# Kernel optimization log

Measured on AMD Instinct MI355X. Metric: run time of the kernel, lower is better.

## Reference

```python
import jax, jax.numpy as jnp
import numpy as np

N_NODES = 100000
N_EDGES = 1600000
IN_C, HID_C, OUT_C = 64, 64, 32


def gcn_conv(x, edge_index, W, b, n_nodes):
    """PyG GCNConv: add self-loops, symmetric norm, x @ W, scatter-add, + bias."""
    loop = jnp.arange(n_nodes, dtype=edge_index.dtype)
    src = jnp.concatenate([edge_index[0], loop])  # [E + N]
    dst = jnp.concatenate([edge_index[1], loop])
    # degree on destination (col) including self-loops -> deg >= 1
    deg = jax.ops.segment_sum(jnp.ones_like(dst, dtype=x.dtype), dst,
                              num_segments=n_nodes)
    dinv = jax.lax.rsqrt(deg)  # deg >= 1, no inf handling needed
    norm = dinv[src] * dinv[dst]  # [E + N]
    h = x @ W  # [N, C_out] -- transform first (small GEMM), then propagate
    msg = h[src] * norm[:, None]  # gather, memory-bound
    out = jax.ops.segment_sum(msg, dst, num_segments=n_nodes)  # scatter-add
    return out + b


def setup_inputs() -> dict:
    key = jax.random.key(0)
    k1, k2, k3, k4, k5 = jax.random.split(key, 5)
    x = jax.random.normal(k1, (N_NODES, IN_C), dtype=jnp.float32)
    edge_index = jax.random.randint(k2, (2, N_EDGES), 0, N_NODES, dtype=jnp.int64)
    s1 = 1.0 / np.sqrt(IN_C)
    s2 = 1.0 / np.sqrt(HID_C)
    W1 = jax.random.uniform(k3, (IN_C, HID_C), jnp.float32, -s1, s1)
    b1 = jnp.zeros((HID_C,), jnp.float32)
    W2 = jax.random.uniform(k4, (HID_C, OUT_C), jnp.float32, -s2, s2)
    b2 = jnp.zeros((OUT_C,), jnp.float32)
    return {"x": x, "edge_index": edge_index, "W1": W1, "b1": b1,
            "W2": W2, "b2": b2}


def reference(x, edge_index, W1, b1, W2, b2):
    n = x.shape[0]
    h = gcn_conv(x, edge_index, W1, b1, n)
    h = jax.nn.relu(h)
    out = gcn_conv(h, edge_index, W2, b2, n)
    return out
```

## Files before the change

kernel.cpp:

```cpp
#include <hip/hip_runtime.h>
#include <hip/hip_fp16.h>
#include <cstdint>
#include <cstddef>


#define CHUNK 4096
#define BKN 256
#define BKN_SHIFT 8
#define NCH_MAX 512
#define SCAP2 5120

__device__ __forceinline__ int load_edge(const int* e32, int idx, int is64) {
  if (is64) return (int)((const long long*)e32)[idx];
  return e32[idx];
}

__device__ __forceinline__ int detect_is64_block(const int* e32, int* s_tmp) {
  const int t = threadIdx.x;
  if (t < 64) {
    int v = e32[2 * t + 1];
    unsigned long long b = __ballot(v != 0);
    if (t == 0) *s_tmp = (b == 0ULL);
  }
  __syncthreads();
  return *s_tmp;
}

__global__ void k_histA(const int* __restrict__ e32, int E, int* __restrict__ histM,
                        int NBUCK) {
  __shared__ int lh[NCH_MAX];
  __shared__ int s_is64;
  const int c = blockIdx.x;
  const int t = threadIdx.x;
  const int is64 = detect_is64_block(e32, &s_is64);
  for (int i = t; i < NBUCK; i += 256) lh[i] = 0;
  __syncthreads();
  const int beg = c * CHUNK;
  const int n = min(CHUNK, E - beg);
  for (int i = t; i < n; i += 256) {
    int d = load_edge(e32, E + beg + i, is64);
    atomicAdd(&lh[d >> BKN_SHIFT], 1);
  }
  __syncthreads();
  for (int i = t; i < NBUCK; i += 256) histM[(size_t)c * NBUCK + i] = lh[i];
}

__device__ __forceinline__ void block_scan512(int* sh, int t) {
  for (int off = 1; off < 512; off <<= 1) {
    int i0 = t, i1 = t + 256;
    int v0 = sh[i0] + ((i0 >= off) ? sh[i0 - off] : 0);
    int v1 = sh[i1] + ((i1 >= off) ? sh[i1 - off] : 0);
    __syncthreads();
    sh[i0] = v0;
    sh[i1] = v1;
    __syncthreads();
  }
}

__global__ void k_colscanA(int* __restrict__ histM, int* __restrict__ btot,
                           int NCH, int NBUCK) {
  __shared__ int sh[NCH_MAX];
  const int b = blockIdx.x;
  const int t = threadIdx.x;
  for (int i = t; i < NCH_MAX; i += 256)
    sh[i] = (i < NCH) ? histM[(size_t)i * NBUCK + b] : 0;
  __syncthreads();
  block_scan512(sh, t);
  for (int i = t; i < NCH; i += 256)
    histM[(size_t)i * NBUCK + b] = (i == 0) ? 0 : sh[i - 1];
  if (t == 0) btot[b] = sh[NCH_MAX - 1];
}

__global__ void k_bscan(const int* __restrict__ btot, int* __restrict__ bbase,
                        int* __restrict__ rowptr, __half* __restrict__ h1,
                        __half* __restrict__ g1, __half* __restrict__ h2,
                        int NBUCK, int N, int E) {
  __shared__ int sh[NCH_MAX];
  const int t = threadIdx.x;
  sh[t] = (t < NBUCK) ? btot[t] : 0;
  sh[t + 256] = (t + 256 < NBUCK) ? btot[t + 256] : 0;
  __syncthreads();
  block_scan512(sh, t);
  for (int i = t; i < NBUCK; i += 256) bbase[i] = (i == 0) ? 0 : sh[i - 1];
  if (t == 0) { bbase[NBUCK] = E; rowptr[N] = E; }
  if (t < 64) {
    h1[(size_t)N * 64 + t] = __float2half(0.f);
    g1[(size_t)N * 64 + t] = __float2half(0.f);
    if (t < 32) h2[(size_t)N * 32 + t] = __float2half(0.f);
  }
}

__global__ void k_scatter(const int* __restrict__ e32, int E, const int* __restrict__ histM,
                          const int* __restrict__ bbase, int NBUCK,
                          unsigned int* __restrict__ raw) {
  __shared__ int lcur[NCH_MAX];
  __shared__ int s_is64;
  const int c = blockIdx.x;
  const int t = threadIdx.x;
  const int is64 = detect_is64_block(e32, &s_is64);
  for (int i = t; i < NBUCK; i += 256)
    lcur[i] = histM[(size_t)c * NBUCK + i] + bbase[i];
  __syncthreads();
  const int beg = c * CHUNK;
  const int cnt = min(CHUNK, E - beg);
  for (int i = t; i < cnt; i += 256) {
    int s = load_edge(e32, beg + i, is64);
    int d = load_edge(e32, E + beg + i, is64);
    int pos = atomicAdd(&lcur[d >> BKN_SHIFT], 1);
    raw[pos] = ((unsigned int)(d & (BKN - 1)) << 23) | (unsigned int)s;
  }
}

__global__ void k_sort(const unsigned int* __restrict__ raw, const int* __restrict__ bbase,
                       int* __restrict__ rec, int* __restrict__ rowptr,
                       float* __restrict__ dinv, int N) {
  __shared__ int srec[SCAP2];
  __shared__ int sh[BKN];
  const int b = blockIdx.x;
  const int t = threadIdx.x;
  const int nodebase = b << BKN_SHIFT;
  const int base = bbase[b];
  const int end = bbase[b + 1];
  const int count = end - base;
  sh[t] = 0;
  __syncthreads();
  for (int i = t; i < count; i += 256) atomicAdd(&sh[raw[base + i] >> 23], 1);
  __syncthreads();
  const int deg = sh[t];
  for (int off = 1; off < 256; off <<= 1) {
    int add = (t >= off) ? sh[t - off] : 0;
    __syncthreads();
    sh[t] += add;
    __syncthreads();
  }
  const int excl = sh[t] - deg;
  const int n = nodebase + t;
  if (n < N) {
    rowptr[n] = base + excl;
    dinv[n] = rsqrtf((float)deg + 1.0f);
  }
  __syncthreads();
  sh[t] = excl;
  __syncthreads();
  if (count <= SCAP2) {
    for (int i = t; i < count; i += 256) {
      unsigned int r = raw[base + i];
      int pos = atomicAdd(&sh[r >> 23], 1);
      srec[pos] = (int)(r & 0x7FFFFFu);
    }
    __syncthreads();
    for (int i = t; i < count; i += 256) rec[base + i] = srec[i];
  } else {
    for (int i = t; i < count; i += 256) {
      unsigned int r = raw[base + i];
      int pos = atomicAdd(&sh[r >> 23], 1);
      rec[base + pos] = (int)(r & 0x7FFFFFu);
    }
  }
}

template <int CIN, int COUT, bool IN16>
__global__ void k_gemm(const void* __restrict__ Xv, const float* __restrict__ W,
                       const float* __restrict__ dinv, __half* __restrict__ H, int N) {
  constexpr int Q = COUT / 4;
  constexpr int NODES = 256 / Q;
  __shared__ float4 Ws[CIN * Q];
  __shared__ float Xs[NODES][CIN + 1];
  const int t = threadIdx.x;
  const int nodebase = blockIdx.x * NODES;

  const float4* W4 = (const float4*)W;
#pragma unroll
  for (int i = t; i < CIN * Q; i += 256) Ws[i] = W4[i];

  if (IN16) {
    const __half2* X2 = (const __half2*)Xv;
#pragma unroll
    for (int i = t; i < NODES * (CIN / 2); i += 256) {
      int r = i / (CIN / 2);
      int k2 = i % (CIN / 2);
      int gr = nodebase + r;
      if (gr > N - 1) gr = N - 1;
      float2 f = __half22float2(X2[(size_t)gr * (CIN / 2) + k2]);
      Xs[r][k2 * 2 + 0] = f.x;
      Xs[r][k2 * 2 + 1] = f.y;
    }
  } else {
    const float4* X4 = (const float4*)Xv;
#pragma unroll
    for (int i = t; i < NODES * (CIN / 4); i += 256) {
      int r = i / (CIN / 4);
      int k4 = i % (CIN / 4);
      int gr = nodebase + r;
      if (gr > N - 1) gr = N - 1;
      float4 v = X4[(size_t)gr * (CIN / 4) + k4];
      Xs[r][k4 * 4 + 0] = v.x;
      Xs[r][k4 * 4 + 1] = v.y;
      Xs[r][k4 * 4 + 2] = v.z;
      Xs[r][k4 * 4 + 3] = v.w;
    }
  }
  __syncthreads();

  const int q = t % Q;
  const int nl = t / Q;
  const int n = nodebase + nl;
  float4 acc = make_float4(0.f, 0.f, 0.f, 0.f);
#pragma unroll 4
  for (int k = 0; k < CIN; ++k) {
    float xv = Xs[nl][k];
    float4 wv = Ws[k * Q + q];
    acc.x = fmaf(xv, wv.x, acc.x);
    acc.y = fmaf(xv, wv.y, acc.y);
    acc.z = fmaf(xv, wv.z, acc.z);
    acc.w = fmaf(xv, wv.w, acc.w);
  }
  if (n < N) {
    float dn = dinv[n];
    __half2* H2 = (__half2*)H;
    H2[(size_t)n * (COUT / 2) + 2 * q + 0] = __floats2half2_rn(acc.x * dn, acc.y * dn);
    H2[(size_t)n * (COUT / 2) + 2 * q + 1] = __floats2half2_rn(acc.z * dn, acc.w * dn);
  }
}

__device__ __forceinline__ void acc_row(float4 hv, float2& a0, float2& a1,
                                        float2& a2, float2& a3) {
  union { float f; __half2 h; } c0, c1, c2, c3;
  c0.f = hv.x; c1.f = hv.y; c2.f = hv.z; c3.f = hv.w;
  float2 f0 = __half22float2(c0.h), f1 = __half22float2(c1.h);
  float2 f2 = __half22float2(c2.h), f3 = __half22float2(c3.h);
  a0.x += f0.x; a0.y += f0.y;
  a1.x += f1.x; a1.y += f1.y;
  a2.x += f2.x; a2.y += f2.y;
  a3.x += f3.x; a3.y += f3.y;
}

#define RED2(v, m) { v.x += __shfl_xor(v.x, m); v.y += __shfl_xor(v.y, m); }

__global__ void k_prop64(const __half2* __restrict__ H2, const int* __restrict__ rec,
                         const int* __restrict__ rowptr, const float* __restrict__ dinv,
                         const float* __restrict__ bias, __half* __restrict__ out, int N) {
  const int lane = threadIdx.x & 63;
  const int wave = threadIdx.x >> 6;
  const int n = blockIdx.x * 16 + wave * 4 + (lane >> 4);
  if (n >= N) return;
  const int g = (lane & 15) >> 3;
  const int l8 = lane & 7;
  const float di = dinv[n];
  const int beg = rowptr[n];
  const int end = rowptr[n + 1];
  const float4* H4 = (const float4*)H2;
  float2 a0 = {0.f, 0.f}, a1 = {0.f, 0.f}, a2 = {0.f, 0.f}, a3 = {0.f, 0.f};
  acc_row(H4[(size_t)(g == 0 ? n : N) * 8 + l8], a0, a1, a2, a3);
  for (int e = beg + g; e < end; e += 16) {
    int s0 = rec[e];
    int s1 = (e + 2  < end) ? rec[e + 2]  : N;
    int s2 = (e + 4  < end) ? rec[e + 4]  : N;
    int s3 = (e + 6  < end) ? rec[e + 6]  : N;
    int s4 = (e + 8  < end) ? rec[e + 8]  : N;
    int s5 = (e + 10 < end) ? rec[e + 10] : N;
    int s6 = (e + 12 < end) ? rec[e + 12] : N;
    int s7 = (e + 14 < end) ? rec[e + 14] : N;
    acc_row(H4[(size_t)s0 * 8 + l8], a0, a1, a2, a3);
    acc_row(H4[(size_t)s1 * 8 + l8], a0, a1, a2, a3);
    acc_row(H4[(size_t)s2 * 8 + l8], a0, a1, a2, a3);
    acc_row(H4[(size_t)s3 * 8 + l8], a0, a1, a2, a3);
    acc_row(H4[(size_t)s4 * 8 + l8], a0, a1, a2, a3);
    acc_row(H4[(size_t)s5 * 8 + l8], a0, a1, a2, a3);
    acc_row(H4[(size_t)s6 * 8 + l8], a0, a1, a2, a3);
    acc_row(H4[(size_t)s7 * 8 + l8], a0, a1, a2, a3);
  }
  RED2(a0, 8)  RED2(a1, 8)  RED2(a2, 8)  RED2(a3, 8)
  if (g) return;
  const float4* B4 = (const float4*)bias;
  float4 b0 = B4[l8 * 2 + 0], b1 = B4[l8 * 2 + 1];
  union { float4 f4; __half2 h2[4]; } st;
  st.h2[0] = __floats2half2_rn(fmaxf(fmaf(a0.x, di, b0.x), 0.f),
                               fmaxf(fmaf(a0.y, di, b0.y), 0.f));
  st.h2[1] = __floats2half2_rn(fmaxf(fmaf(a1.x, di, b0.z), 0.f),
                               fmaxf(fmaf(a1.y, di, b0.w), 0.f));
  st.h2[2] = __floats2half2_rn(fmaxf(fmaf(a2.x, di, b1.x), 0.f),
                               fmaxf(fmaf(a2.y, di, b1.y), 0.f));
  st.h2[3] = __floats2half2_rn(fmaxf(fmaf(a3.x, di, b1.z), 0.f),
                               fmaxf(fmaf(a3.y, di, b1.w), 0.f));
  ((float4*)out)[(size_t)n * 8 + l8] = st.f4;
}

__global__ void k_prop32(const __half2* __restrict__ H2, const int* __restrict__ rec,
                         const int* __restrict__ rowptr, const float* __restrict__ dinv,
                         const float* __restrict__ bias, float* __restrict__ out, int N) {
  const int lane = threadIdx.x & 63;
  const int wave = threadIdx.x >> 6;
  const int n = blockIdx.x * 32 + wave * 8 + (lane >> 3);
  if (n >= N) return;
  const int g = (lane & 7) >> 2;
  const int l4 = lane & 3;
  const float di = dinv[n];
  const int beg = rowptr[n];
  const int end = rowptr[n + 1];
  const float4* H4 = (const float4*)H2;
  float2 a0 = {0.f, 0.f}, a1 = {0.f, 0.f}, a2 = {0.f, 0.f}, a3 = {0.f, 0.f};
  acc_row(H4[(size_t)(g == 0 ? n : N) * 4 + l4], a0, a1, a2, a3);
  for (int e = beg + g; e < end; e += 16) {
    int s0 = rec[e];
    int s1 = (e + 2  < end) ? rec[e + 2]  : N;
    int s2 = (e + 4  < end) ? rec[e + 4]  : N;
    int s3 = (e + 6  < end) ? rec[e + 6]  : N;
    int s4 = (e + 8  < end) ? rec[e + 8]  : N;
    int s5 = (e + 10 < end) ? rec[e + 10] : N;
    int s6 = (e + 12 < end) ? rec[e + 12] : N;
    int s7 = (e + 14 < end) ? rec[e + 14] : N;
    acc_row(H4[(size_t)s0 * 4 + l4], a0, a1, a2, a3);
    acc_row(H4[(size_t)s1 * 4 + l4], a0, a1, a2, a3);
    acc_row(H4[(size_t)s2 * 4 + l4], a0, a1, a2, a3);
    acc_row(H4[(size_t)s3 * 4 + l4], a0, a1, a2, a3);
    acc_row(H4[(size_t)s4 * 4 + l4], a0, a1, a2, a3);
    acc_row(H4[(size_t)s5 * 4 + l4], a0, a1, a2, a3);
    acc_row(H4[(size_t)s6 * 4 + l4], a0, a1, a2, a3);
    acc_row(H4[(size_t)s7 * 4 + l4], a0, a1, a2, a3);
  }
  RED2(a0, 4)  RED2(a1, 4)  RED2(a2, 4)  RED2(a3, 4)
  if (g) return;
  const float4* B4 = (const float4*)bias;
  float4 b0 = B4[l4 * 2 + 0], b1 = B4[l4 * 2 + 1];
  ((float4*)out)[(size_t)n * 8 + l4 * 2 + 0] =
      make_float4(fmaf(a0.x, di, b0.x), fmaf(a0.y, di, b0.y),
                  fmaf(a1.x, di, b0.z), fmaf(a1.y, di, b0.w));
  ((float4*)out)[(size_t)n * 8 + l4 * 2 + 1] =
      make_float4(fmaf(a2.x, di, b1.x), fmaf(a2.y, di, b1.y),
                  fmaf(a3.x, di, b1.z), fmaf(a3.y, di, b1.w));
}

extern "C" void kernel_launch(void* const* d_in, const int* in_sizes, int n_in,
                              void* d_out, int out_size, void* d_ws, size_t ws_size,
                              hipStream_t stream) {
  (void)n_in; (void)out_size; (void)ws_size;
  const float* x = (const float*)d_in[0];
  const int* edges = (const int*)d_in[1];
  const float* W1 = (const float*)d_in[2];
  const float* b1 = (const float*)d_in[3];
  const float* W2 = (const float*)d_in[4];
  const float* b2 = (const float*)d_in[5];

  const int N = in_sizes[0] / 64;
  const int E = in_sizes[1] / 2;
  const int NCH = (E + CHUNK - 1) / CHUNK;
  const int NBUCK = (N + BKN - 1) / BKN;

  char* ws = (char*)d_ws;
  size_t off = 0;
  auto carve = [&](size_t bytes) -> void* {
    void* p = ws + off;
    off = (off + bytes + 255) & ~(size_t)255;
    return p;
  };
  int* rowptr        = (int*)carve((size_t)(N + 1) * 4);
  float* dinv        = (float*)carve((size_t)N * 4);
  int* btot          = (int*)carve((size_t)NBUCK * 4);
  int* bbase         = (int*)carve((size_t)(NBUCK + 1) * 4);
  int* histM         = (int*)carve((size_t)NCH * NBUCK * 4);
  unsigned int* raw  = (unsigned int*)carve((size_t)E * 4);
  int* rec           = (int*)carve(((size_t)E + 64) * 4);
  __half* h1         = (__half*)carve((size_t)(N + 1) * 64 * 2);
  __half* g1         = (__half*)carve((size_t)(N + 1) * 64 * 2);
  __half* h2         = (__half*)carve((size_t)(N + 1) * 32 * 2);

  k_histA<<<NCH, 256, 0, stream>>>(edges, E, histM, NBUCK);
  k_colscanA<<<NBUCK, 256, 0, stream>>>(histM, btot, NCH, NBUCK);
  k_bscan<<<1, 256, 0, stream>>>(btot, bbase, rowptr, h1, g1, h2, NBUCK, N, E);
  k_scatter<<<NCH, 256, 0, stream>>>(edges, E, histM, bbase, NBUCK, raw);
  k_sort<<<NBUCK, 256, 0, stream>>>(raw, bbase, rec, rowptr, dinv, N);

  k_gemm<64, 64, false><<<(N + 15) / 16, 256, 0, stream>>>(x, W1, dinv, h1, N);
  k_prop64<<<(N + 15) / 16, 256, 0, stream>>>((const __half2*)h1, rec, rowptr, dinv,
                                              b1, g1, N);
  k_gemm<64, 32, true><<<(N + 31) / 32, 256, 0, stream>>>(g1, W2, dinv, h2, N);
  k_prop32<<<(N + 31) / 32, 256, 0, stream>>>((const __half2*)h2, rec, rowptr, dinv,
                                              b2, (float*)d_out, N);
}
```

Measured before the change: 133.1 us.

## Fuse layer-2 GEMM into layer-1 propagation epilogue via shared memory

The layer-1 aggregation kernel now applies bias and ReLU, stages each node's 64-wide hidden row in shared memory, and multiplies it by W2 (also loaded into shared memory) to write the dinv-scaled layer-2 input directly. This removes the fp16 g1 intermediate buffer, its write and reread, and one kernel launch. In exchange, every block loads W2 into LDS, adds a block barrier, and out-of-range threads are clamped to the last node, so they do redundant work and write duplicate values. The hidden activations also stay in fp32 instead of being rounded to fp16 before the second GEMM.

```diff
diff --git a/kernel.cpp b/kernel.cpp
--- a/kernel.cpp
+++ b/kernel.cpp
@@ -73,8 +73,7 @@
 
 __global__ void k_bscan(const int* __restrict__ btot, int* __restrict__ bbase,
                         int* __restrict__ rowptr, __half* __restrict__ h1,
-                        __half* __restrict__ g1, __half* __restrict__ h2,
-                        int NBUCK, int N, int E) {
+                        __half* __restrict__ h2, int NBUCK, int N, int E) {
   __shared__ int sh[NCH_MAX];
   const int t = threadIdx.x;
   sh[t] = (t < NBUCK) ? btot[t] : 0;
@@ -85,7 +84,6 @@
   if (t == 0) { bbase[NBUCK] = E; rowptr[N] = E; }
   if (t < 64) {
     h1[(size_t)N * 64 + t] = __float2half(0.f);
-    g1[(size_t)N * 64 + t] = __float2half(0.f);
     if (t < 32) h2[(size_t)N * 32 + t] = __float2half(0.f);
   }
 }
@@ -159,8 +157,8 @@
   }
 }
 
-template <int CIN, int COUT, bool IN16>
-__global__ void k_gemm(const void* __restrict__ Xv, const float* __restrict__ W,
+template <int CIN, int COUT>
+__global__ void k_gemm(const float* __restrict__ Xv, const float* __restrict__ W,
                        const float* __restrict__ dinv, __half* __restrict__ H, int N) {
   constexpr int Q = COUT / 4;
   constexpr int NODES = 256 / Q;
@@ -173,32 +171,18 @@
 #pragma unroll
   for (int i = t; i < CIN * Q; i += 256) Ws[i] = W4[i];
 
-  if (IN16) {
-    const __half2* X2 = (const __half2*)Xv;
+  const float4* X4 = (const float4*)Xv;
 #pragma unroll
-    for (int i = t; i < NODES * (CIN / 2); i += 256) {
-      int r = i / (CIN / 2);
-      int k2 = i % (CIN / 2);
-      int gr = nodebase + r;
-      if (gr > N - 1) gr = N - 1;
-      float2 f = __half22float2(X2[(size_t)gr * (CIN / 2) + k2]);
-      Xs[r][k2 * 2 + 0] = f.x;
-      Xs[r][k2 * 2 + 1] = f.y;
-    }
-  } else {
-    const float4* X4 = (const float4*)Xv;
-#pragma unroll
-    for (int i = t; i < NODES * (CIN / 4); i += 256) {
-      int r = i / (CIN / 4);
-      int k4 = i % (CIN / 4);
-      int gr = nodebase + r;
-      if (gr > N - 1) gr = N - 1;
-      float4 v = X4[(size_t)gr * (CIN / 4) + k4];
-      Xs[r][k4 * 4 + 0] = v.x;
-      Xs[r][k4 * 4 + 1] = v.y;
-      Xs[r][k4 * 4 + 2] = v.z;
-      Xs[r][k4 * 4 + 3] = v.w;
-    }
+  for (int i = t; i < NODES * (CIN / 4); i += 256) {
+    int r = i / (CIN / 4);
+    int k4 = i % (CIN / 4);
+    int gr = nodebase + r;
+    if (gr > N - 1) gr = N - 1;
+    float4 v = X4[(size_t)gr * (CIN / 4) + k4];
+    Xs[r][k4 * 4 + 0] = v.x;
+    Xs[r][k4 * 4 + 1] = v.y;
+    Xs[r][k4 * 4 + 2] = v.z;
+    Xs[r][k4 * 4 + 3] = v.w;
   }
   __syncthreads();
 
@@ -237,13 +221,23 @@
 
 #define RED2(v, m) { v.x += __shfl_xor(v.x, m); v.y += __shfl_xor(v.y, m); }
 
-__global__ void k_prop64(const __half2* __restrict__ H2, const int* __restrict__ rec,
-                         const int* __restrict__ rowptr, const float* __restrict__ dinv,
-                         const float* __restrict__ bias, __half* __restrict__ out, int N) {
-  const int lane = threadIdx.x & 63;
-  const int wave = threadIdx.x >> 6;
-  const int n = blockIdx.x * 16 + wave * 4 + (lane >> 4);
-  if (n >= N) return;
+__global__ void k_prop64f(const __half2* __restrict__ H2, const int* __restrict__ rec,
+                          const int* __restrict__ rowptr, const float* __restrict__ dinv,
+                          const float* __restrict__ b1, const float* __restrict__ W2,
+                          __half* __restrict__ h2, int N) {
+  __shared__ float2 W2p[64 * 16];
+  __shared__ float g1buf[4][4][68];
+  const int t = threadIdx.x;
+  const int lane = t & 63;
+  const int wave = t >> 6;
+  for (int i = t; i < 64 * 16; i += 256) {
+    int c = i >> 4, k = i & 15;
+    W2p[i] = make_float2(W2[c * 32 + k], W2[c * 32 + 16 + k]);
+  }
+
+  const int nl = lane >> 4;
+  int n = blockIdx.x * 16 + wave * 4 + nl;
+  if (n > N - 1) n = N - 1;
   const int g = (lane & 15) >> 3;
   const int l8 = lane & 7;
   const float di = dinv[n];
@@ -271,19 +265,39 @@
     acc_row(H4[(size_t)s7 * 8 + l8], a0, a1, a2, a3);
   }
   RED2(a0, 8)  RED2(a1, 8)  RED2(a2, 8)  RED2(a3, 8)
-  if (g) return;
-  const float4* B4 = (const float4*)bias;
-  float4 b0 = B4[l8 * 2 + 0], b1 = B4[l8 * 2 + 1];
-  union { float4 f4; __half2 h2[4]; } st;
-  st.h2[0] = __floats2half2_rn(fmaxf(fmaf(a0.x, di, b0.x), 0.f),
-                               fmaxf(fmaf(a0.y, di, b0.y), 0.f));
-  st.h2[1] = __floats2half2_rn(fmaxf(fmaf(a1.x, di, b0.z), 0.f),
-                               fmaxf(fmaf(a1.y, di, b0.w), 0.f));
-  st.h2[2] = __floats2half2_rn(fmaxf(fmaf(a2.x, di, b1.x), 0.f),
-                               fmaxf(fmaf(a2.y, di, b1.y), 0.f));
-  st.h2[3] = __floats2half2_rn(fmaxf(fmaf(a3.x, di, b1.z), 0.f),
-                               fmaxf(fmaf(a3.y, di, b1.w), 0.f));
-  ((float4*)out)[(size_t)n * 8 + l8] = st.f4;
+
+  const float4* B4 = (const float4*)b1;
+  float4 bb0 = B4[l8 * 2 + 0], bb1 = B4[l8 * 2 + 1];
+  if (g == 0) {
+    float4 r0 = make_float4(fmaxf(fmaf(a0.x, di, bb0.x), 0.f),
+                            fmaxf(fmaf(a0.y, di, bb0.y), 0.f),
+                            fmaxf(fmaf(a1.x, di, bb0.z), 0.f),
+                            fmaxf(fmaf(a1.y, di, bb0.w), 0.f));
+    float4 r1 = make_float4(fmaxf(fmaf(a2.x, di, bb1.x), 0.f),
+                            fmaxf(fmaf(a2.y, di, bb1.y), 0.f),
+                            fmaxf(fmaf(a3.x, di, bb1.z), 0.f),
+                            fmaxf(fmaf(a3.y, di, bb1.w), 0.f));
+    *(float4*)&g1buf[wave][nl][l8 * 8 + 0] = r0;
+    *(float4*)&g1buf[wave][nl][l8 * 8 + 4] = r1;
+  }
+  __syncthreads();
+
+  const int k = lane & 15;
+  float o0 = 0.f, o1 = 0.f;
+#pragma unroll
+  for (int c4 = 0; c4 < 16; ++c4) {
+    float4 r = *(const float4*)&g1buf[wave][nl][c4 * 4];
+    float2 w0 = W2p[(c4 * 4 + 0) * 16 + k];
+    float2 w1 = W2p[(c4 * 4 + 1) * 16 + k];
+    float2 w2 = W2p[(c4 * 4 + 2) * 16 + k];
+    float2 w3 = W2p[(c4 * 4 + 3) * 16 + k];
+    o0 = fmaf(r.x, w0.x, o0); o1 = fmaf(r.x, w0.y, o1);
+    o0 = fmaf(r.y, w1.x, o0); o1 = fmaf(r.y, w1.y, o1);
+    o0 = fmaf(r.z, w2.x, o0); o1 = fmaf(r.z, w2.y, o1);
+    o0 = fmaf(r.w, w3.x, o0); o1 = fmaf(r.w, w3.y, o1);
+  }
+  h2[(size_t)n * 32 + k]      = __float2half(o0 * di);
+  h2[(size_t)n * 32 + k + 16] = __float2half(o1 * di);
 }
 
 __global__ void k_prop32(const __half2* __restrict__ H2, const int* __restrict__ rec,
@@ -362,19 +376,17 @@
   unsigned int* raw  = (unsigned int*)carve((size_t)E * 4);
   int* rec           = (int*)carve(((size_t)E + 64) * 4);
   __half* h1         = (__half*)carve((size_t)(N + 1) * 64 * 2);
-  __half* g1         = (__half*)carve((size_t)(N + 1) * 64 * 2);
   __half* h2         = (__half*)carve((size_t)(N + 1) * 32 * 2);
 
   k_histA<<<NCH, 256, 0, stream>>>(edges, E, histM, NBUCK);
   k_colscanA<<<NBUCK, 256, 0, stream>>>(histM, btot, NCH, NBUCK);
-  k_bscan<<<1, 256, 0, stream>>>(btot, bbase, rowptr, h1, g1, h2, NBUCK, N, E);
+  k_bscan<<<1, 256, 0, stream>>>(btot, bbase, rowptr, h1, h2, NBUCK, N, E);
   k_scatter<<<NCH, 256, 0, stream>>>(edges, E, histM, bbase, NBUCK, raw);
   k_sort<<<NBUCK, 256, 0, stream>>>(raw, bbase, rec, rowptr, dinv, N);
 
-  k_gemm<64, 64, false><<<(N + 15) / 16, 256, 0, stream>>>(x, W1, dinv, h1, N);
-  k_prop64<<<(N + 15) / 16, 256, 0, stream>>>((const __half2*)h1, rec, rowptr, dinv,
-                                              b1, g1, N);
-  k_gemm<64, 32, true><<<(N + 31) / 32, 256, 0, stream>>>(g1, W2, dinv, h2, N);
+  k_gemm<64, 64><<<(N + 15) / 16, 256, 0, stream>>>(x, W1, dinv, h1, N);
+  k_prop64f<<<(N + 15) / 16, 256, 0, stream>>>((const __half2*)h1, rec, rowptr,
+                                               dinv, b1, W2, h2, N);
   k_prop32<<<(N + 31) / 32, 256, 0, stream>>>((const __half2*)h2, rec, rowptr, dinv,
                                               b2, (float*)d_out, N);
 }
```

New measurement: 123.5 us. -7.2%, faster.
